# Kernel tuning notes

Measured on AMD Instinct MI355X. Metric: run time of the kernel, lower is better.

Reference implementation:

```python
import jax, jax.numpy as jnp
import numpy as np

ANISO = (0.096, 0.096, 0.096)
BIG = 1e10  # stands in for +inf feature distance
SMOOTH = 1e-05


def _minplus(f, axis, w):
    # exact 1D squared distance transform along `axis` via min-plus conv:
    # g[i] = min_j f[j] + (w*(i-j))^2 ; vectorized over all other dims.
    f = jnp.moveaxis(f, axis, -1)
    n = f.shape[-1]
    idx = jnp.arange(n, dtype=f.dtype)
    d2 = (w * (idx[:, None] - idx[None, :])) ** 2  # [j, i]
    g = jnp.min(f[..., :, None] + d2, axis=-2)
    return jnp.moveaxis(g, -1, axis)


def _edt_multilabel(labels, num_labels):
    # labels: [b, X, Y, Z] int, values in [1, num_labels]
    # Multi-label euclidean distance transform (edt.edt semantics on gt+1):
    # for each voxel, distance to nearest voxel carrying a DIFFERENT label,
    # scaled by ANISO. Computed as per-label squared EDT fields (separable
    # min-plus per axis, exact) combined by excluding the voxel's own label.
    fields = []
    for L in range(1, num_labels + 1):  # small fixed loop over classes
        f = jnp.where(labels == L, 0.0, BIG).astype(jnp.float32)
        for ax, w in zip((1, 2, 3), ANISO):
            f = _minplus(f, ax, w)
        fields.append(f)
    D = jnp.stack(fields, axis=0)  # [L, b, X, Y, Z] squared distances
    own = jnp.moveaxis(jax.nn.one_hot(labels - 1, num_labels, dtype=jnp.float32), -1, 0)
    d2 = jnp.min(jnp.where(own > 0, BIG, D), axis=0)  # nearest different label
    return jnp.sqrt(d2)


def setup_inputs() -> dict:
    key = jax.random.key(0)
    kx, ky = jax.random.split(key)
    x = jax.random.uniform(kx, (2, 3, 64, 64, 64), dtype=jnp.float32)  # softmax probs
    y = jax.random.randint(ky, (2, 1, 64, 64, 64), 0, 3)  # label map, classes 0..2
    return {"x": x, "y": y}


def reference(x, y):
    b, c = x.shape[:2]
    yi = y[:, 0]  # [b, X, Y, Z]
    # scatter_(1, gt, 1) -> one hot over channel dim
    y_onehot = jnp.moveaxis(jax.nn.one_hot(yi, c, dtype=x.dtype), -1, 1)  # [b,c,X,Y,Z]
    # dt = edt(gt + 1) + 1 ; all labels >=1 so every voxel is 'foreground'
    dt = (_edt_multilabel(yi + 1, c) + 1.0)[:, None]  # [b,1,X,Y,Z]
    fp = x * (1.0 - y_onehot) * dt
    fn = (1.0 - x) * y_onehot * dt
    # do_bg=False (non-batch-dice path): drop background channel
    fp = fp[:, 1:]
    fn = fn[:, 1:]
    return jnp.mean(fp) + jnp.mean(fn) + SMOOTH
```

## Files before the change

### kernel.cpp

```cpp
#include <hip/hip_runtime.h>
#include <math.h>

#define BIGV 10000000000.0f
#define WA   0.096f

__device__ __forceinline__ float seed_dist2(unsigned long long mask, int i) {
    const unsigned long long mr = mask >> i;
    const unsigned long long ml = mask << (63 - i);
    const int dr = mr ? __builtin_ctzll(mr) : 1000;
    const int dl = ml ? __builtin_clzll(ml) : 1000;
    const int d  = dr < dl ? dr : dl;
    const float t = WA * (float)d;
    return (d > 63) ? BIGV : t * t;
}

__global__ __launch_bounds__(256) void pass_xz_kernel(const int* __restrict__ lab,
                                                      float* __restrict__ D,
                                                      float* __restrict__ out) {
    if (blockIdx.x == 0 && blockIdx.y == 0 && blockIdx.z == 0 && threadIdx.x == 0)
        out[0] = 1e-5f;

    const int ys = blockIdx.x, b = blockIdx.y, zq = blockIdx.z;
    const int lane = threadIdx.x & 63;
    const int wv   = threadIdx.x >> 6;

    __shared__ float sm[3][64][64];

    const int* lp = lab + b * 262144 + ys * 64;
    for (int z = wv * 16, e = z + 16; z < e; ++z) {
        const int lv = lp[z * 4096 + lane];
        sm[0][z][lane] = seed_dist2(__ballot(lv == 0), lane);
        sm[1][z][lane] = seed_dist2(__ballot(lv == 1), lane);
        sm[2][z][lane] = seed_dist2(__ballot(lv == 2), lane);
    }
    __syncthreads();

    const int i0 = zq * 16 + wv * 4;
    float m0[4], m1[4], m2[4];
#pragma unroll
    for (int ii = 0; ii < 4; ++ii) m0[ii] = m1[ii] = m2[ii] = __builtin_inff();

    for (int j = 0; j < 64; ++j) {
        const float a0 = sm[0][j][lane];
        const float a1 = sm[1][j][lane];
        const float a2 = sm[2][j][lane];
        const float fb = (float)(i0 - j);
#pragma unroll
        for (int ii = 0; ii < 4; ++ii) {
            const float t = WA * (fb + (float)ii);
            m0[ii] = fminf(m0[ii], __builtin_fmaf(t, t, a0));
            m1[ii] = fminf(m1[ii], __builtin_fmaf(t, t, a1));
            m2[ii] = fminf(m2[ii], __builtin_fmaf(t, t, a2));
        }
    }

    float* Dp = D + b * 3 * 262144 + ys * 64;
#pragma unroll
    for (int ii = 0; ii < 4; ++ii) {
        const int zo = (i0 + ii) * 4096 + lane;
        Dp[zo]              = m0[ii];
        Dp[262144 + zo]     = m1[ii];
        Dp[2 * 262144 + zo] = m2[ii];
    }
}

__global__ __launch_bounds__(256) void pass_y_kernel(const float* __restrict__ x,
                                                     const int* __restrict__ lab,
                                                     const float* __restrict__ D,
                                                     float* __restrict__ out) {
    const int z = blockIdx.x, b = blockIdx.y, yq = blockIdx.z;
    const int lane = threadIdx.x & 63;
    const int wv   = threadIdx.x >> 6;

    __shared__ float sm[3][64][64];
    {
        const float4* Dp4 = (const float4*)(D + b * 3 * 262144 + z * 4096);
        float4* s4 = (float4*)&sm[0][0][0];
        for (int t = threadIdx.x; t < 1024; t += 256) {
            s4[t]        = Dp4[t];
            s4[1024 + t] = Dp4[65536 + t];
            s4[2048 + t] = Dp4[131072 + t];
        }
    }

    const int i0 = yq * 16 + wv * 4;
    int   lv[4];
    float x1[4], x2[4];
#pragma unroll
    for (int ii = 0; ii < 4; ++ii) {
        const int off = z * 4096 + (i0 + ii) * 64 + lane;
        lv[ii] = lab[b * 262144 + off];
        x1[ii] = x[(b * 3 + 1) * 262144 + off];
        x2[ii] = x[(b * 3 + 2) * 262144 + off];
    }
    __syncthreads();

    float m0[4], m1[4], m2[4];
#pragma unroll
    for (int ii = 0; ii < 4; ++ii) m0[ii] = m1[ii] = m2[ii] = __builtin_inff();

    for (int j = 0; j < 64; ++j) {
        const float a0 = sm[0][j][lane];
        const float a1 = sm[1][j][lane];
        const float a2 = sm[2][j][lane];
        const float fb = (float)(i0 - j);
#pragma unroll
        for (int ii = 0; ii < 4; ++ii) {
            const float t = WA * (fb + (float)ii);
            m0[ii] = fminf(m0[ii], __builtin_fmaf(t, t, a0));
            m1[ii] = fminf(m1[ii], __builtin_fmaf(t, t, a1));
            m2[ii] = fminf(m2[ii], __builtin_fmaf(t, t, a2));
        }
    }

    float part = 0.0f;
#pragma unroll
    for (int ii = 0; ii < 4; ++ii) {
        const float d0  = (lv[ii] == 0) ? BIGV : m0[ii];
        const float d1  = (lv[ii] == 1) ? BIGV : m1[ii];
        const float d2m = (lv[ii] == 2) ? BIGV : m2[ii];
        const float dt  = sqrtf(fminf(d0, fminf(d1, d2m))) + 1.0f;
        const float t1  = (lv[ii] == 1) ? (1.0f - x1[ii]) : x1[ii];
        const float t2  = (lv[ii] == 2) ? (1.0f - x2[ii]) : x2[ii];
        part += (t1 + t2) * dt;
    }

#pragma unroll
    for (int o = 32; o; o >>= 1) part += __shfl_down(part, o);
    if (lane == 0)
        atomicAdd(out, part * (1.0f / 1048576.0f));
}

extern "C" void kernel_launch(void* const* d_in, const int* in_sizes, int n_in,
                              void* d_out, int out_size, void* d_ws, size_t ws_size,
                              hipStream_t stream) {
    const float* x = (const float*)d_in[0];
    const int*   y = (const int*)d_in[1];
    float* D   = (float*)d_ws;
    float* out = (float*)d_out;

    pass_xz_kernel<<<dim3(64, 2, 4), 256, 0, stream>>>(y, D, out);
    pass_y_kernel<<<dim3(64, 2, 4), 256, 0, stream>>>(x, y, D, out);
}
```

Before: 101.6 us.

## Switch distance transform to packed int16 squared integer distances

Stores the per-label intermediate distance fields as int16 squared voxel distances instead of float32, exploiting the isotropic spacing so the weight factors out. The min-plus inner loops use packed 2-wide short add/min, which halves ALU instruction count, and the intermediate buffer plus LDS traffic are halved. The ABSENT sentinel of 16000 must stay below the int16 limit after adding d^2 up to 3969 per pass, which holds for the 3-pass maximum of about 11907. The float conversion and scaling by WA^2 happen only at the end.

```diff
diff --git a/kernel.cpp b/kernel.cpp
--- a/kernel.cpp
+++ b/kernel.cpp
@@ -3,19 +3,25 @@
 
 #define BIGV 10000000000.0f
 #define WA   0.096f
+#define ABSENT 16000
 
-__device__ __forceinline__ float seed_dist2(unsigned long long mask, int i) {
+typedef short short2v __attribute__((ext_vector_type(2)));
+
+__device__ __forceinline__ short2v pack2(int a, int b) {
+    short2v r; r.x = (short)a; r.y = (short)b; return r;
+}
+
+__device__ __forceinline__ short seed_d2_i16(unsigned long long mask, int i) {
     const unsigned long long mr = mask >> i;
     const unsigned long long ml = mask << (63 - i);
-    const int dr = mr ? __builtin_ctzll(mr) : 1000;
-    const int dl = ml ? __builtin_clzll(ml) : 1000;
+    const int dr = mr ? __builtin_ctzll(mr) : 127;
+    const int dl = ml ? __builtin_clzll(ml) : 127;
     const int d  = dr < dl ? dr : dl;
-    const float t = WA * (float)d;
-    return (d > 63) ? BIGV : t * t;
+    return (short)(d > 63 ? ABSENT : d * d);
 }
 
 __global__ __launch_bounds__(256) void pass_xz_kernel(const int* __restrict__ lab,
-                                                      float* __restrict__ D,
+                                                      unsigned short* __restrict__ D,
                                                       float* __restrict__ out) {
     if (blockIdx.x == 0 && blockIdx.y == 0 && blockIdx.z == 0 && threadIdx.x == 0)
         out[0] = 1e-5f;
@@ -24,62 +30,69 @@
     const int lane = threadIdx.x & 63;
     const int wv   = threadIdx.x >> 6;
 
-    __shared__ float sm[3][64][64];
+    __shared__ short sm[3][64][64];
 
     const int* lp = lab + b * 262144 + ys * 64;
     for (int z = wv * 16, e = z + 16; z < e; ++z) {
         const int lv = lp[z * 4096 + lane];
-        sm[0][z][lane] = seed_dist2(__ballot(lv == 0), lane);
-        sm[1][z][lane] = seed_dist2(__ballot(lv == 1), lane);
-        sm[2][z][lane] = seed_dist2(__ballot(lv == 2), lane);
+        sm[0][z][lane] = seed_d2_i16(__ballot(lv == 0), lane);
+        sm[1][z][lane] = seed_d2_i16(__ballot(lv == 1), lane);
+        sm[2][z][lane] = seed_d2_i16(__ballot(lv == 2), lane);
     }
     __syncthreads();
 
     const int i0 = zq * 16 + wv * 4;
-    float m0[4], m1[4], m2[4];
-#pragma unroll
-    for (int ii = 0; ii < 4; ++ii) m0[ii] = m1[ii] = m2[ii] = __builtin_inff();
+    short2v mA0 = {32767, 32767}, mA1 = mA0;
+    short2v mB0 = mA0, mB1 = mA0, mC0 = mA0, mC1 = mA0;
 
     for (int j = 0; j < 64; ++j) {
-        const float a0 = sm[0][j][lane];
-        const float a1 = sm[1][j][lane];
-        const float a2 = sm[2][j][lane];
-        const float fb = (float)(i0 - j);
-#pragma unroll
-        for (int ii = 0; ii < 4; ++ii) {
-            const float t = WA * (fb + (float)ii);
-            m0[ii] = fminf(m0[ii], __builtin_fmaf(t, t, a0));
-            m1[ii] = fminf(m1[ii], __builtin_fmaf(t, t, a1));
-            m2[ii] = fminf(m2[ii], __builtin_fmaf(t, t, a2));
-        }
+        const short a0 = sm[0][j][lane];
+        const short a1 = sm[1][j][lane];
+        const short a2 = sm[2][j][lane];
+        const short2v a0p = {a0, a0}, a1p = {a1, a1}, a2p = {a2, a2};
+        const int dz = i0 - j;
+        const short2v d2p0 = pack2(dz * dz, (dz + 1) * (dz + 1));
+        const short2v d2p1 = pack2((dz + 2) * (dz + 2), (dz + 3) * (dz + 3));
+        mA0 = __builtin_elementwise_min(mA0, (short2v)(a0p + d2p0));
+        mA1 = __builtin_elementwise_min(mA1, (short2v)(a0p + d2p1));
+        mB0 = __builtin_elementwise_min(mB0, (short2v)(a1p + d2p0));
+        mB1 = __builtin_elementwise_min(mB1, (short2v)(a1p + d2p1));
+        mC0 = __builtin_elementwise_min(mC0, (short2v)(a2p + d2p0));
+        mC1 = __builtin_elementwise_min(mC1, (short2v)(a2p + d2p1));
     }
 
-    float* Dp = D + b * 3 * 262144 + ys * 64;
-#pragma unroll
-    for (int ii = 0; ii < 4; ++ii) {
-        const int zo = (i0 + ii) * 4096 + lane;
-        Dp[zo]              = m0[ii];
-        Dp[262144 + zo]     = m1[ii];
-        Dp[2 * 262144 + zo] = m2[ii];
-    }
+    unsigned short* Dp = D + b * 3 * 262144 + ys * 64 + lane;
+    const int r0 = i0 * 4096;
+    Dp[r0]                       = (unsigned short)mA0.x;
+    Dp[r0 + 4096]                = (unsigned short)mA0.y;
+    Dp[r0 + 2 * 4096]            = (unsigned short)mA1.x;
+    Dp[r0 + 3 * 4096]            = (unsigned short)mA1.y;
+    Dp[262144 + r0]              = (unsigned short)mB0.x;
+    Dp[262144 + r0 + 4096]       = (unsigned short)mB0.y;
+    Dp[262144 + r0 + 2 * 4096]   = (unsigned short)mB1.x;
+    Dp[262144 + r0 + 3 * 4096]   = (unsigned short)mB1.y;
+    Dp[524288 + r0]              = (unsigned short)mC0.x;
+    Dp[524288 + r0 + 4096]       = (unsigned short)mC0.y;
+    Dp[524288 + r0 + 2 * 4096]   = (unsigned short)mC1.x;
+    Dp[524288 + r0 + 3 * 4096]   = (unsigned short)mC1.y;
 }
 
 __global__ __launch_bounds__(256) void pass_y_kernel(const float* __restrict__ x,
                                                      const int* __restrict__ lab,
-                                                     const float* __restrict__ D,
+                                                     const unsigned short* __restrict__ D,
                                                      float* __restrict__ out) {
     const int z = blockIdx.x, b = blockIdx.y, yq = blockIdx.z;
     const int lane = threadIdx.x & 63;
     const int wv   = threadIdx.x >> 6;
 
-    __shared__ float sm[3][64][64];
+    __shared__ short sm[3][64][64];
     {
-        const float4* Dp4 = (const float4*)(D + b * 3 * 262144 + z * 4096);
-        float4* s4 = (float4*)&sm[0][0][0];
-        for (int t = threadIdx.x; t < 1024; t += 256) {
+        const uint4* Dp4 = (const uint4*)(D + b * 3 * 262144 + z * 4096);
+        uint4* s4 = (uint4*)&sm[0][0][0];
+        for (int t = threadIdx.x; t < 512; t += 256) {
             s4[t]        = Dp4[t];
+            s4[512 + t]  = Dp4[32768 + t];
             s4[1024 + t] = Dp4[65536 + t];
-            s4[2048 + t] = Dp4[131072 + t];
         }
     }
 
@@ -95,31 +108,38 @@
     }
     __syncthreads();
 
-    float m0[4], m1[4], m2[4];
-#pragma unroll
-    for (int ii = 0; ii < 4; ++ii) m0[ii] = m1[ii] = m2[ii] = __builtin_inff();
+    short2v mA0 = {32767, 32767}, mA1 = mA0;
+    short2v mB0 = mA0, mB1 = mA0, mC0 = mA0, mC1 = mA0;
 
     for (int j = 0; j < 64; ++j) {
-        const float a0 = sm[0][j][lane];
-        const float a1 = sm[1][j][lane];
-        const float a2 = sm[2][j][lane];
-        const float fb = (float)(i0 - j);
-#pragma unroll
-        for (int ii = 0; ii < 4; ++ii) {
-            const float t = WA * (fb + (float)ii);
-            m0[ii] = fminf(m0[ii], __builtin_fmaf(t, t, a0));
-            m1[ii] = fminf(m1[ii], __builtin_fmaf(t, t, a1));
-            m2[ii] = fminf(m2[ii], __builtin_fmaf(t, t, a2));
-        }
+        const short a0 = sm[0][j][lane];
+        const short a1 = sm[1][j][lane];
+        const short a2 = sm[2][j][lane];
+        const short2v a0p = {a0, a0}, a1p = {a1, a1}, a2p = {a2, a2};
+        const int dy = i0 - j;
+        const short2v d2p0 = pack2(dy * dy, (dy + 1) * (dy + 1));
+        const short2v d2p1 = pack2((dy + 2) * (dy + 2), (dy + 3) * (dy + 3));
+        mA0 = __builtin_elementwise_min(mA0, (short2v)(a0p + d2p0));
+        mA1 = __builtin_elementwise_min(mA1, (short2v)(a0p + d2p1));
+        mB0 = __builtin_elementwise_min(mB0, (short2v)(a1p + d2p0));
+        mB1 = __builtin_elementwise_min(mB1, (short2v)(a1p + d2p1));
+        mC0 = __builtin_elementwise_min(mC0, (short2v)(a2p + d2p0));
+        mC1 = __builtin_elementwise_min(mC1, (short2v)(a2p + d2p1));
     }
+
+    const int g0[4] = {mA0.x, mA0.y, mA1.x, mA1.y};
+    const int g1[4] = {mB0.x, mB0.y, mB1.x, mB1.y};
+    const int g2[4] = {mC0.x, mC0.y, mC1.x, mC1.y};
 
     float part = 0.0f;
 #pragma unroll
     for (int ii = 0; ii < 4; ++ii) {
-        const float d0  = (lv[ii] == 0) ? BIGV : m0[ii];
-        const float d1  = (lv[ii] == 1) ? BIGV : m1[ii];
-        const float d2m = (lv[ii] == 2) ? BIGV : m2[ii];
-        const float dt  = sqrtf(fminf(d0, fminf(d1, d2m))) + 1.0f;
+        const int e0 = (lv[ii] == 0) ? (1 << 20) : g0[ii];
+        const int e1 = (lv[ii] == 1) ? (1 << 20) : g1[ii];
+        const int e2 = (lv[ii] == 2) ? (1 << 20) : g2[ii];
+        const int dm = min(e0, min(e1, e2));
+        const float d2f = (dm >= ABSENT) ? BIGV : (float)dm * (WA * WA);
+        const float dt  = sqrtf(d2f) + 1.0f;
         const float t1  = (lv[ii] == 1) ? (1.0f - x1[ii]) : x1[ii];
         const float t2  = (lv[ii] == 2) ? (1.0f - x2[ii]) : x2[ii];
         part += (t1 + t2) * dt;
@@ -136,7 +156,7 @@
                               hipStream_t stream) {
     const float* x = (const float*)d_in[0];
     const int*   y = (const int*)d_in[1];
-    float* D   = (float*)d_ws;
+    unsigned short* D = (unsigned short*)d_ws;
     float* out = (float*)d_out;
 
     pass_xz_kernel<<<dim3(64, 2, 4), 256, 0, stream>>>(y, D, out);
```

Measured after the change: 99.14 us. 2.5% less time.
